# Kernel optimization log

Hardware: AMD Instinct MI355X
Metric: run time of the kernel (lower is better)

Reference implementation:

```python
import jax, jax.numpy as jnp
import numpy as np

N_SRC, N_TGT, K, L, C_OUT = 16384, 16384, 16, 128, 2
E = N_TGT * K
MIN_VAR = 1e-3   # adf.keep_variance_fn min variance (applied in Dropout)
DROP_P = 0.2
INV_SQRT2 = np.float32(1.0 / np.sqrt(2.0))
INV_SQRT2PI = np.float32(1.0 / np.sqrt(2.0 * np.pi))


def setup_inputs() -> dict:
    key = jax.random.key(0)
    ks = jax.random.split(key, 12)
    pos_source = jax.random.uniform(ks[0], (N_SRC, 3), jnp.float32)
    pos_target = jax.random.uniform(ks[1], (N_TGT, 3), jnp.float32)
    latents = jax.random.normal(ks[2], (N_SRC, L), jnp.float32)
    var = jax.random.uniform(ks[3], (N_SRC, L), jnp.float32)
    # KNN-style edge list: each target has K source neighbors
    row = jnp.repeat(jnp.arange(N_TGT, dtype=jnp.int32), K)          # [E] target idx
    col = jax.random.randint(ks[4], (E,), 0, N_SRC, jnp.int32)       # [E] source idx
    occupancies = jax.random.randint(ks[5], (N_TGT,), 0, 2, jnp.int32)
    # fixed inverted-dropout mask (deterministic stand-in for adf.Dropout training mask)
    drop_mask = (jax.random.uniform(ks[6], (E, L)) >= DROP_P).astype(jnp.float32) / (1.0 - DROP_P)
    def init_w(k, sh):
        return jax.random.normal(k, sh, jnp.float32) * np.float32(1.0 / np.sqrt(sh[-1]))
    W_in = init_w(ks[7], (L, L + 3)); b_in = jnp.zeros((L,), jnp.float32)
    W1 = init_w(ks[8], (L, L)); b1 = jnp.zeros((L,), jnp.float32)
    W2 = init_w(ks[9], (L, L)); b2 = jnp.zeros((L,), jnp.float32)
    W_out = init_w(ks[10], (C_OUT, L)); b_out = jnp.zeros((C_OUT,), jnp.float32)
    return dict(pos_source=pos_source, pos_target=pos_target, latents=latents, var=var,
                drop_mask=drop_mask, W_in=W_in, b_in=b_in, W1=W1, b1=b1, W2=W2, b2=b2,
                W_out=W_out, b_out=b_out, row=row, col=col, occupancies=occupancies)


def _adf_linear(m, v, W, b):
    # ADF Linear: mean -> affine; variance -> through squared weights, no bias
    return m @ W.T + b, v @ (W * W).T


def _adf_relu(m, v):
    # ADF ReLU moment matching (Gast & Roth); clamp var for sqrt stability
    v = jnp.maximum(v, 1e-6)
    std = jnp.sqrt(v)
    r = m / std
    cdf = 0.5 * (1.0 + jax.lax.erf(r * INV_SQRT2))
    pdf = jnp.exp(-0.5 * r * r) * INV_SQRT2PI
    m_out = m * cdf + std * pdf
    v_out = (m * m + v) * cdf + m * std * pdf - m_out * m_out
    return m_out, v_out


def reference(pos_source, pos_target, latents, var, drop_mask, W_in, b_in, W1, b1, W2, b2, W_out, b_out, row, col, occupancies):
    pos_rel = pos_target[row] - pos_source[col]                    # [E,3]
    m = jnp.concatenate([latents[col], pos_rel], axis=1)           # [E,L+3]
    v = jnp.concatenate([var[col], pos_rel], axis=1)               # [E,L+3] (faithful: pos_rel reused as 'variance')
    m, v = _adf_linear(m, v, W_in, b_in)
    for W, b in ((W1, b1), (W2, b2)):
        m, v = _adf_relu(m, v)
        m, v = _adf_linear(m, v, W, b)
    # ADF dropout with keep_variance_fn
    m = m * drop_mask
    v = v * drop_mask * drop_mask + MIN_VAR
    m, v = _adf_linear(m, v, W_out, b_out)                         # [E,2]
    preds = m[:, 0]
    aleatoric = jnp.abs(v[:, 0]).mean()
    occ_gt = occupancies[row].astype(jnp.float32)
    # stable binary_cross_entropy_with_logits, mean reduction
    recons_loss = jnp.mean(jnp.maximum(preds, 0.0) - preds * occ_gt + jnp.log1p(jnp.exp(-jnp.abs(preds))))
    return preds, aleatoric, recons_loss, occ_gt
```

## Files before the change

### kernel.cpp

```cpp
#include <hip/hip_runtime.h>
#include <math.h>

#define E_TOT 262144
#define N_SRC 16384
#define LDIM  128
#define XPB   272
#define MIN_VARF 0.001f
#define INV_SQRT2PIF 0.3989422804014327f
#define EPB   128
#define NBLK  (E_TOT / EPB)

typedef _Float16 half8  __attribute__((ext_vector_type(8)));
typedef __fp16   fp16x2 __attribute__((ext_vector_type(2)));
typedef float    f32x4  __attribute__((ext_vector_type(4)));
typedef float    f32x2  __attribute__((ext_vector_type(2)));
typedef unsigned int uint2v __attribute__((ext_vector_type(2)));

#define BIAS_OFF  256
#define WOUT_OFF  1792
#define BOUT_OFF  2816
#define PK_L0     4096
#define PK_L1     45056
#define PK_L2     77824
#define PART_OFF  110592
#define LAT16_OFF 131072
#define VAR16_OFF (LAT16_OFF + N_SRC * LDIM * 2)
#define WS_NEED   (VAR16_OFF + N_SRC * LDIM * 2)

__device__ __forceinline__ unsigned int pkrtz(float a, float b) {
    union { fp16x2 h; unsigned int u; } z;
    z.h = __builtin_amdgcn_cvt_pkrtz(a, b);
    return z.u;
}
__device__ __forceinline__ half8 to_h8(f32x4 a, f32x4 b) {
    union { half8 h; unsigned int u[4]; } z;
    z.u[0] = pkrtz(a[0], a[1]); z.u[1] = pkrtz(a[2], a[3]);
    z.u[2] = pkrtz(b[0], b[1]); z.u[3] = pkrtz(b[2], b[3]);
    return z.h;
}

__device__ __forceinline__ void adf_relu(float& m, float& v) {
    float vv = fmaxf(v, 1e-6f);
    float is = __builtin_amdgcn_rsqf(vv);
    float sd = vv * is;
    float r  = m * is;
    float qq = 0.5f * r * r;
    float e  = __expf(-qq);
    float sp = sd * e * INV_SQRT2PIF;
    const float P = 0.23165247f;
    float t  = __builtin_amdgcn_rcpf(fmaf(fabsf(r), P, 1.0f));
    float poly = t * fmaf(t, fmaf(t, fmaf(t, fmaf(t, 1.061405429f, -1.453152027f),
                                          1.421413741f), -0.284496736f), 0.254829592f);
    float erfa = fmaf(-poly, e, 1.0f);
    float cdf  = fmaf(copysignf(0.5f, r), erfa, 0.5f);
    float mo = fmaf(m, cdf, sp);
    float vo = fmaf(fmaf(m, m, vv), cdf, fmaf(m, sp, -mo * mo));
    m = mo; v = vo;
}

__global__ void prep_pack(const float* __restrict__ latents, const float* __restrict__ varr,
                          char* __restrict__ ws)
{
    int idx = blockIdx.x * 256 + threadIdx.x;
    const int half = idx >> 18;
    const int j    = idx & 262143;
    const float* src = (half ? varr : latents) + (long)j * 8;
    char* dst = ws + (half ? VAR16_OFF : LAT16_OFF) + (long)j * 16;
    f32x4 a = *(const f32x4*)(src);
    f32x4 b = *(const f32x4*)(src + 4);
    half8 hv;
#pragma unroll
    for (int k = 0; k < 4; ++k) { hv[k] = (_Float16)a[k]; hv[k + 4] = (_Float16)b[k]; }
    *(half8*)dst = hv;
}

__global__ void prep(const float* __restrict__ W_in, const float* __restrict__ b_in,
                     const float* __restrict__ W1,   const float* __restrict__ b1,
                     const float* __restrict__ W2,   const float* __restrict__ b2,
                     const float* __restrict__ W_out,const float* __restrict__ b_out,
                     char* __restrict__ ws)
{
    int idx = blockIdx.x * 256 + threadIdx.x;
    if (idx < 6656) {
        const float* W; int Kfull; long dstoff; int entry;
        if (idx < 2560)      { entry = idx;        W = W_in; Kfull = 131; dstoff = PK_L0; }
        else if (idx < 4608) { entry = idx - 2560; W = W1;   Kfull = 128; dstoff = PK_L1; }
        else                 { entry = idx - 4608; W = W2;   Kfull = 128; dstoff = PK_L2; }
        int ks   = entry >> 9;
        int rest = entry & 511;
        int t    = rest >> 6;
        int lane = rest & 63;
        int rowi = t * 16 + (lane & 15);
        int k0   = ks * 32 + (lane >> 4) * 8;
        half8 hv;
#pragma unroll
        for (int j = 0; j < 8; ++j) {
            int k = k0 + j;
            hv[j] = (_Float16)((k < Kfull) ? W[rowi * Kfull + k] : 0.0f);
        }
        *(half8*)(ws + dstoff + (long)entry * 16) = hv;
    } else if (idx < 6656 + 384) {
        int j = idx - 6656; int layer = j >> 7; int pidx = j & 127;
        int gg = pidx >> 5, t = (pidx >> 2) & 7, r = pidx & 3;
        int n = t * 16 + gg * 4 + r;
        const float* b = layer == 0 ? b_in : (layer == 1 ? b1 : b2);
        ((float*)(ws + BIAS_OFF))[layer * 128 + pidx] = b[n];
    } else if (idx < 6656 + 384 + 256) {
        int j = idx - 6656 - 384; int path = j >> 7; int pidx = j & 127;
        int gg = pidx >> 5, t = (pidx >> 2) & 7, r = pidx & 3;
        int n = t * 16 + gg * 4 + r;
        float v = W_out[n];
        if (path) v = v * v;
        ((float*)(ws + WOUT_OFF))[path * 128 + pidx] = v;
    } else if (idx == 6656 + 384 + 256) {
        ((float*)(ws + BOUT_OFF))[0] = b_out[0];
    }
}

__device__ __forceinline__ void epi_store(const f32x4* am, const f32x4* av, const f32x4* bp,
                                          char* xmb, char* xvb, int rowb, int g8)
{
#pragma unroll
    for (int t = 0; t < 8; ++t) {
        f32x4 b4 = bp[t];
        float m0 = am[t][0] + b4[0], m1 = am[t][1] + b4[1];
        float m2 = am[t][2] + b4[2], m3 = am[t][3] + b4[3];
        float v0 = av[t][0], v1 = av[t][1], v2 = av[t][2], v3 = av[t][3];
        adf_relu(m0, v0); adf_relu(m1, v1); adf_relu(m2, v2); adf_relu(m3, v3);
        uint2v sm = {pkrtz(m0, m1), pkrtz(m2, m3)};
        uint2v sv = {pkrtz(v0, v1), pkrtz(v2, v3)};
        *(uint2v*)(xmb + rowb + t * 32 + g8) = sm;
        *(uint2v*)(xvb + rowb + t * 32 + g8) = sv;
    }
}

template <bool PACKED>
__global__ void __launch_bounds__(256, 2)
interp_main(const float* __restrict__ pos_source, const float* __restrict__ pos_target,
            const float* __restrict__ latents,    const float* __restrict__ varr,
            const float* __restrict__ drop_mask,
            const int* __restrict__ row, const int* __restrict__ col, const int* __restrict__ occ,
            float* __restrict__ out, char* __restrict__ ws)
{
    __shared__ __align__(16) short Xm[EPB][XPB / 2];
    __shared__ __align__(16) short Xv[EPB][XPB / 2];
    __shared__ float wred[4][2];

    const int tid  = threadIdx.x;
    const int lane = tid & 63;
    const int w    = tid >> 6;
    const int q    = lane & 15;
    const int g    = lane >> 4;
    const int g8   = g * 8;
    const int er0  = w * 32 + q;
    const int er1  = er0 + 16;
    const int ge0  = blockIdx.x * EPB + er0;
    const int ge1  = ge0 + 16;
    char* xmb = (char*)&Xm[0][0];
    char* xvb = (char*)&Xv[0][0];

    const int c0 = col[ge0], c1 = col[ge1];
    const int r0 = row[ge0], r1 = row[ge1];
    const float occf0 = (float)occ[r0];
    const float occf1 = (float)occ[r1];
    const float px0 = pos_target[r0 * 3 + 0] - pos_source[c0 * 3 + 0];
    const float py0 = pos_target[r0 * 3 + 1] - pos_source[c0 * 3 + 1];
    const float pz0 = pos_target[r0 * 3 + 2] - pos_source[c0 * 3 + 2];
    const float px1 = pos_target[r1 * 3 + 0] - pos_source[c1 * 3 + 0];
    const float py1 = pos_target[r1 * 3 + 1] - pos_source[c1 * 3 + 1];
    const float pz1 = pos_target[r1 * 3 + 2] - pos_source[c1 * 3 + 2];

    f32x4 acm0[8], acv0[8], acm1[8], acv1[8];
    const f32x4 zz = {0.0f, 0.0f, 0.0f, 0.0f};
#pragma unroll
    for (int t = 0; t < 8; ++t) { acm0[t] = zz; acv0[t] = zz; acm1[t] = zz; acv1[t] = zz; }

    {
        const char*  pk  = ws + PK_L0 + lane * 16;
        const char*  l16 = ws + LAT16_OFF;
        const char*  v16 = ws + VAR16_OFF;
        const float* lm0 = latents + (long)c0 * LDIM;
        const float* lv0 = varr    + (long)c0 * LDIM;
        const float* lm1 = latents + (long)c1 * LDIM;
        const float* lv1 = varr    + (long)c1 * LDIM;
#pragma unroll
        for (int ks = 0; ks < 4; ++ks) {
            half8 bm0, bv0, bm1, bv1;
            if (PACKED) {
                const long o0 = (long)c0 * 256 + ks * 64 + g8 * 2;
                const long o1 = (long)c1 * 256 + ks * 64 + g8 * 2;
                bm0 = *(const half8*)(l16 + o0);
                bv0 = *(const half8*)(v16 + o0);
                bm1 = *(const half8*)(l16 + o1);
                bv1 = *(const half8*)(v16 + o1);
            } else {
                const f32x4* a0 = (const f32x4*)(lm0 + ks * 32 + g8);
                const f32x4* s0 = (const f32x4*)(lv0 + ks * 32 + g8);
                const f32x4* a1 = (const f32x4*)(lm1 + ks * 32 + g8);
                const f32x4* s1 = (const f32x4*)(lv1 + ks * 32 + g8);
                bm0 = to_h8(a0[0], a0[1]);
                bv0 = to_h8(s0[0], s0[1]);
                bm1 = to_h8(a1[0], a1[1]);
                bv1 = to_h8(s1[0], s1[1]);
            }
            const char* pmk = pk + ks * 8192;
#pragma unroll
            for (int t = 0; t < 8; ++t) {
                half8 am = *(const half8*)(pmk + t * 1024);
                half8 av = am * am;
                acm0[t] = __builtin_amdgcn_mfma_f32_16x16x32_f16(am, bm0, acm0[t], 0, 0, 0);
                acm1[t] = __builtin_amdgcn_mfma_f32_16x16x32_f16(am, bm1, acm1[t], 0, 0, 0);
                acv0[t] = __builtin_amdgcn_mfma_f32_16x16x32_f16(av, bv0, acv0[t], 0, 0, 0);
                acv1[t] = __builtin_amdgcn_mfma_f32_16x16x32_f16(av, bv1, acv1[t], 0, 0, 0);
            }
        }
        half8 bp0 = {(_Float16)0.f, (_Float16)0.f, (_Float16)0.f, (_Float16)0.f,
                     (_Float16)0.f, (_Float16)0.f, (_Float16)0.f, (_Float16)0.f};
        half8 bp1 = bp0;
        if (g == 0) {
            bp0[0] = (_Float16)px0; bp0[1] = (_Float16)py0; bp0[2] = (_Float16)pz0;
            bp1[0] = (_Float16)px1; bp1[1] = (_Float16)py1; bp1[2] = (_Float16)pz1;
        }
        const char* pmk = pk + 4 * 8192;
#pragma unroll
        for (int t = 0; t < 8; ++t) {
            half8 am = *(const half8*)(pmk + t * 1024);
            half8 av = am * am;
            acm0[t] = __builtin_amdgcn_mfma_f32_16x16x32_f16(am, bp0, acm0[t], 0, 0, 0);
            acm1[t] = __builtin_amdgcn_mfma_f32_16x16x32_f16(am, bp1, acm1[t], 0, 0, 0);
            acv0[t] = __builtin_amdgcn_mfma_f32_16x16x32_f16(av, bp0, acv0[t], 0, 0, 0);
            acv1[t] = __builtin_amdgcn_mfma_f32_16x16x32_f16(av, bp1, acv1[t], 0, 0, 0);
        }
        const f32x4* bp = (const f32x4*)(ws + BIAS_OFF) + g * 8;
        epi_store(acm0, acv0, bp, xmb, xvb, er0 * XPB, g8);
        epi_store(acm1, acv1, bp, xmb, xvb, er1 * XPB, g8);
    }

    for (int layer = 1; layer < 3; ++layer) {
        const char* pk = ws + (layer == 1 ? PK_L1 : PK_L2) + lane * 16;
#pragma unroll
        for (int t = 0; t < 8; ++t) { acm0[t] = zz; acv0[t] = zz; acm1[t] = zz; acv1[t] = zz; }
#pragma unroll
        for (int ks = 0; ks < 4; ++ks) {
            half8 bm0 = *(const half8*)(xmb + er0 * XPB + ks * 64 + g * 16);
            half8 bv0 = *(const half8*)(xvb + er0 * XPB + ks * 64 + g * 16);
            half8 bm1 = *(const half8*)(xmb + er1 * XPB + ks * 64 + g * 16);
            half8 bv1 = *(const half8*)(xvb + er1 * XPB + ks * 64 + g * 16);
            const char* pmk = pk + ks * 8192;
#pragma unroll
            for (int t = 0; t < 8; ++t) {
                half8 am = *(const half8*)(pmk + t * 1024);
                half8 av = am * am;
                acm0[t] = __builtin_amdgcn_mfma_f32_16x16x32_f16(am, bm0, acm0[t], 0, 0, 0);
                acm1[t] = __builtin_amdgcn_mfma_f32_16x16x32_f16(am, bm1, acm1[t], 0, 0, 0);
                acv0[t] = __builtin_amdgcn_mfma_f32_16x16x32_f16(av, bv0, acv0[t], 0, 0, 0);
                acv1[t] = __builtin_amdgcn_mfma_f32_16x16x32_f16(av, bv1, acv1[t], 0, 0, 0);
            }
        }
        if (layer == 1) {
            const f32x4* bp = (const f32x4*)(ws + BIAS_OFF) + 32 + g * 8;
            epi_store(acm0, acv0, bp, xmb, xvb, er0 * XPB, g8);
            epi_store(acm1, acv1, bp, xmb, xvb, er1 * XPB, g8);
        }
    }

    {
        const f32x4* wmp = (const f32x4*)(ws + WOUT_OFF);
        const f32x4* bp  = (const f32x4*)(ws + BIAS_OFF) + 64 + g * 8;
        const f32x4* dm0 = (const f32x4*)(drop_mask + (size_t)ge0 * LDIM) + g;
        const f32x4* dm1 = (const f32x4*)(drop_mask + (size_t)ge1 * LDIM) + g;
        float pm0 = 0.f, pv0 = 0.f, pm1 = 0.f, pv1 = 0.f;
#pragma unroll
        for (int t = 0; t < 8; ++t) {
            f32x4 b4 = bp[t];
            f32x4 w4 = wmp[g * 8 + t];
            f32x4 s4 = wmp[32 + g * 8 + t];
            f32x4 d0 = __builtin_nontemporal_load(dm0 + t * 4);
            f32x4 d1 = __builtin_nontemporal_load(dm1 + t * 4);
#pragma unroll
            for (int j = 0; j < 4; ++j) {
                float m0 = (acm0[t][j] + b4[j]) * d0[j];
                float v0 = acv0[t][j] * d0[j] * d0[j] + MIN_VARF;
                float m1 = (acm1[t][j] + b4[j]) * d1[j];
                float v1 = acv1[t][j] * d1[j] * d1[j] + MIN_VARF;
                pm0 = fmaf(w4[j], m0, pm0); pv0 = fmaf(s4[j], v0, pv0);
                pm1 = fmaf(w4[j], m1, pm1); pv1 = fmaf(s4[j], v1, pv1);
            }
        }
        pm0 += __shfl_xor(pm0, 16, 64); pm0 += __shfl_xor(pm0, 32, 64);
        pv0 += __shfl_xor(pv0, 16, 64); pv0 += __shfl_xor(pv0, 32, 64);
        pm1 += __shfl_xor(pm1, 16, 64); pm1 += __shfl_xor(pm1, 32, 64);
        pv1 += __shfl_xor(pv1, 16, 64); pv1 += __shfl_xor(pv1, 32, 64);
        float bout = *(const float*)(ws + BOUT_OFF);
        float p0 = pm0 + bout;
        float p1 = pm1 + bout;
        if (lane < 16) {
            out[ge0] = p0;            out[ge1] = p1;
            out[E_TOT + 2 + ge0] = occf0;
            out[E_TOT + 2 + ge1] = occf1;
        }
        float a0 = fabsf(p0), a1 = fabsf(p1);
        float loss = fmaxf(p0, 0.f) - p0 * occf0 + __logf(1.0f + __expf(-a0))
                   + fmaxf(p1, 0.f) - p1 * occf1 + __logf(1.0f + __expf(-a1));
        float al = fabsf(pv0) + fabsf(pv1);
#pragma unroll
        for (int off = 1; off < 16; off <<= 1) {
            al   += __shfl_xor(al, off, 64);
            loss += __shfl_xor(loss, off, 64);
        }
        if (lane == 0) { wred[w][0] = al; wred[w][1] = loss; }
    }
    __syncthreads();
    if (tid == 0) {
        f32x2 s;
        s[0] = wred[0][0] + wred[1][0] + wred[2][0] + wred[3][0];
        s[1] = wred[0][1] + wred[1][1] + wred[2][1] + wred[3][1];
        *((f32x2*)(ws + PART_OFF) + blockIdx.x) = s;
    }
}

__global__ void __launch_bounds__(256)
interp_finalize(const char* __restrict__ ws, float* __restrict__ out)
{
    __shared__ float sal[4], sls[4];
    const int tid  = threadIdx.x;
    const int lane = tid & 63;
    const int w    = tid >> 6;
    float al = 0.0f, ls = 0.0f;
    const f32x2* part = (const f32x2*)(ws + PART_OFF);
    for (int i = tid; i < NBLK; i += 256) {
        f32x2 p = part[i];
        al += p[0]; ls += p[1];
    }
#pragma unroll
    for (int off = 1; off < 64; off <<= 1) {
        al += __shfl_xor(al, off, 64);
        ls += __shfl_xor(ls, off, 64);
    }
    if (lane == 0) { sal[w] = al; sls[w] = ls; }
    __syncthreads();
    if (tid == 0) {
        const float inv = 1.0f / (float)E_TOT;
        out[E_TOT]     = (sal[0] + sal[1] + sal[2] + sal[3]) * inv;
        out[E_TOT + 1] = (sls[0] + sls[1] + sls[2] + sls[3]) * inv;
    }
}

extern "C" void kernel_launch(void* const* d_in, const int* in_sizes, int n_in,
                              void* d_out, int out_size, void* d_ws, size_t ws_size,
                              hipStream_t stream) {
    (void)in_sizes; (void)n_in; (void)out_size;
    const float* pos_source = (const float*)d_in[0];
    const float* pos_target = (const float*)d_in[1];
    const float* latents    = (const float*)d_in[2];
    const float* varr       = (const float*)d_in[3];
    const float* drop_mask  = (const float*)d_in[4];
    const float* W_in       = (const float*)d_in[5];
    const float* b_in       = (const float*)d_in[6];
    const float* W1         = (const float*)d_in[7];
    const float* b1         = (const float*)d_in[8];
    const float* W2         = (const float*)d_in[9];
    const float* b2         = (const float*)d_in[10];
    const float* W_out      = (const float*)d_in[11];
    const float* b_out      = (const float*)d_in[12];
    const int*   row        = (const int*)d_in[13];
    const int*   col        = (const int*)d_in[14];
    const int*   occ        = (const int*)d_in[15];
    float* out = (float*)d_out;
    char*  ws  = (char*)d_ws;

    const bool packed = (ws_size >= (size_t)WS_NEED);
    prep<<<29, 256, 0, stream>>>(W_in, b_in, W1, b1, W2, b2, W_out, b_out, ws);
    if (packed) {
        prep_pack<<<2048, 256, 0, stream>>>(latents, varr, ws);
        interp_main<true><<<NBLK, 256, 0, stream>>>(
            pos_source, pos_target, latents, varr, drop_mask,
            row, col, occ, out, ws);
    } else {
        interp_main<false><<<NBLK, 256, 0, stream>>>(
            pos_source, pos_target, latents, varr, drop_mask,
            row, col, occ, out, ws);
    }
    interp_finalize<<<1, 256, 0, stream>>>(ws, out);
}
```

Baseline: 148.1 us.

## Keep inter-layer activations in registers instead of LDS, halve edges per wave

Hidden activations no longer make a round trip through LDS between layers. Instead, layers 1 and 2 are given a K-permuted weight packing so that the MFMA accumulator layout of one layer directly forms the B operand of the next, and the packed fp16 results stay in registers. Each wave now handles 16 edges instead of 32, with 64 edges per block, and launch bounds go from 2 to 3 blocks per SM to raise occupancy. This removes the LDS stores, loads and shared memory footprint. In exchange, each weight fragment loaded from global/L2 is reused across half as many MFMAs, so weight traffic per edge doubles.

```diff
diff --git a/kernel.cpp b/kernel.cpp
--- a/kernel.cpp
+++ b/kernel.cpp
@@ -4,10 +4,9 @@
 #define E_TOT 262144
 #define N_SRC 16384
 #define LDIM  128
-#define XPB   272
 #define MIN_VARF 0.001f
 #define INV_SQRT2PIF 0.3989422804014327f
-#define EPB   128
+#define EPB   64
 #define NBLK  (E_TOT / EPB)
 
 typedef _Float16 half8  __attribute__((ext_vector_type(8)));
@@ -19,13 +18,13 @@
 #define BIAS_OFF  256
 #define WOUT_OFF  1792
 #define BOUT_OFF  2816
-#define PK_L0     4096
-#define PK_L1     45056
-#define PK_L2     77824
-#define PART_OFF  110592
-#define LAT16_OFF 131072
-#define VAR16_OFF (LAT16_OFF + N_SRC * LDIM * 2)
-#define WS_NEED   (VAR16_OFF + N_SRC * LDIM * 2)
+#define PART_OFF  4096
+#define PK_L0     36864
+#define PK_L1     77824
+#define PK_L2     110592
+#define LAT16_OFF 143360
+#define VAR16_OFF 4337664
+#define WS_NEED   8531968
 
 __device__ __forceinline__ unsigned int pkrtz(float a, float b) {
     union { fp16x2 h; unsigned int u; } z;
@@ -36,6 +35,11 @@
     union { half8 h; unsigned int u[4]; } z;
     z.u[0] = pkrtz(a[0], a[1]); z.u[1] = pkrtz(a[2], a[3]);
     z.u[2] = pkrtz(b[0], b[1]); z.u[3] = pkrtz(b[2], b[3]);
+    return z.h;
+}
+__device__ __forceinline__ half8 ch_to_h8(uint2v lo, uint2v hi) {
+    union { half8 h; unsigned int u[4]; } z;
+    z.u[0] = lo[0]; z.u[1] = lo[1]; z.u[2] = hi[0]; z.u[3] = hi[1];
     return z.h;
 }
 
@@ -82,21 +86,30 @@
 {
     int idx = blockIdx.x * 256 + threadIdx.x;
     if (idx < 6656) {
-        const float* W; int Kfull; long dstoff; int entry;
-        if (idx < 2560)      { entry = idx;        W = W_in; Kfull = 131; dstoff = PK_L0; }
-        else if (idx < 4608) { entry = idx - 2560; W = W1;   Kfull = 128; dstoff = PK_L1; }
-        else                 { entry = idx - 4608; W = W2;   Kfull = 128; dstoff = PK_L2; }
+        const float* W; long dstoff; int entry; bool lin;
+        if (idx < 2560)      { entry = idx;        W = W_in; dstoff = PK_L0; lin = true;  }
+        else if (idx < 4608) { entry = idx - 2560; W = W1;   dstoff = PK_L1; lin = false; }
+        else                 { entry = idx - 4608; W = W2;   dstoff = PK_L2; lin = false; }
         int ks   = entry >> 9;
         int rest = entry & 511;
         int t    = rest >> 6;
         int lane = rest & 63;
         int rowi = t * 16 + (lane & 15);
-        int k0   = ks * 32 + (lane >> 4) * 8;
+        int gp   = lane >> 4;
         half8 hv;
-#pragma unroll
-        for (int j = 0; j < 8; ++j) {
-            int k = k0 + j;
-            hv[j] = (_Float16)((k < Kfull) ? W[rowi * Kfull + k] : 0.0f);
+        if (lin) {
+            int k0 = ks * 32 + gp * 8;
+#pragma unroll
+            for (int j = 0; j < 8; ++j) {
+                int k = k0 + j;
+                hv[j] = (_Float16)((k < 131) ? W[rowi * 131 + k] : 0.0f);
+            }
+        } else {
+#pragma unroll
+            for (int j = 0; j < 8; ++j) {
+                int k = (2 * ks + (j >= 4 ? 1 : 0)) * 16 + 4 * gp + (j & 3);
+                hv[j] = (_Float16)W[rowi * 128 + k];
+            }
         }
         *(half8*)(ws + dstoff + (long)entry * 16) = hv;
     } else if (idx < 6656 + 384) {
@@ -117,8 +130,8 @@
     }
 }
 
-__device__ __forceinline__ void epi_store(const f32x4* am, const f32x4* av, const f32x4* bp,
-                                          char* xmb, char* xvb, int rowb, int g8)
+__device__ __forceinline__ void epi_reg(const f32x4* am, const f32x4* av, const f32x4* bp,
+                                        uint2v* chm, uint2v* chv)
 {
 #pragma unroll
     for (int t = 0; t < 8; ++t) {
@@ -129,21 +142,18 @@
         adf_relu(m0, v0); adf_relu(m1, v1); adf_relu(m2, v2); adf_relu(m3, v3);
         uint2v sm = {pkrtz(m0, m1), pkrtz(m2, m3)};
         uint2v sv = {pkrtz(v0, v1), pkrtz(v2, v3)};
-        *(uint2v*)(xmb + rowb + t * 32 + g8) = sm;
-        *(uint2v*)(xvb + rowb + t * 32 + g8) = sv;
+        chm[t] = sm; chv[t] = sv;
     }
 }
 
 template <bool PACKED>
-__global__ void __launch_bounds__(256, 2)
+__global__ void __launch_bounds__(256, 3)
 interp_main(const float* __restrict__ pos_source, const float* __restrict__ pos_target,
             const float* __restrict__ latents,    const float* __restrict__ varr,
             const float* __restrict__ drop_mask,
             const int* __restrict__ row, const int* __restrict__ col, const int* __restrict__ occ,
             float* __restrict__ out, char* __restrict__ ws)
 {
-    __shared__ __align__(16) short Xm[EPB][XPB / 2];
-    __shared__ __align__(16) short Xv[EPB][XPB / 2];
     __shared__ float wred[4][2];
 
     const int tid  = threadIdx.x;
@@ -152,157 +162,113 @@
     const int q    = lane & 15;
     const int g    = lane >> 4;
     const int g8   = g * 8;
-    const int er0  = w * 32 + q;
-    const int er1  = er0 + 16;
-    const int ge0  = blockIdx.x * EPB + er0;
-    const int ge1  = ge0 + 16;
-    char* xmb = (char*)&Xm[0][0];
-    char* xvb = (char*)&Xv[0][0];
-
-    const int c0 = col[ge0], c1 = col[ge1];
-    const int r0 = row[ge0], r1 = row[ge1];
-    const float occf0 = (float)occ[r0];
-    const float occf1 = (float)occ[r1];
-    const float px0 = pos_target[r0 * 3 + 0] - pos_source[c0 * 3 + 0];
-    const float py0 = pos_target[r0 * 3 + 1] - pos_source[c0 * 3 + 1];
-    const float pz0 = pos_target[r0 * 3 + 2] - pos_source[c0 * 3 + 2];
-    const float px1 = pos_target[r1 * 3 + 0] - pos_source[c1 * 3 + 0];
-    const float py1 = pos_target[r1 * 3 + 1] - pos_source[c1 * 3 + 1];
-    const float pz1 = pos_target[r1 * 3 + 2] - pos_source[c1 * 3 + 2];
-
-    f32x4 acm0[8], acv0[8], acm1[8], acv1[8];
+    const int er   = w * 16 + q;
+    const int ge   = blockIdx.x * EPB + er;
+    (void)q;
+
+    const int c0 = col[ge];
+    const int r0 = row[ge];
+    const float occf = (float)occ[r0];
+    const float px = pos_target[r0 * 3 + 0] - pos_source[c0 * 3 + 0];
+    const float py = pos_target[r0 * 3 + 1] - pos_source[c0 * 3 + 1];
+    const float pz = pos_target[r0 * 3 + 2] - pos_source[c0 * 3 + 2];
+
+    f32x4 acm[8], acv[8];
     const f32x4 zz = {0.0f, 0.0f, 0.0f, 0.0f};
 #pragma unroll
-    for (int t = 0; t < 8; ++t) { acm0[t] = zz; acv0[t] = zz; acm1[t] = zz; acv1[t] = zz; }
+    for (int t = 0; t < 8; ++t) { acm[t] = zz; acv[t] = zz; }
+
+    uint2v chm[8], chv[8];
 
     {
-        const char*  pk  = ws + PK_L0 + lane * 16;
-        const char*  l16 = ws + LAT16_OFF;
-        const char*  v16 = ws + VAR16_OFF;
-        const float* lm0 = latents + (long)c0 * LDIM;
-        const float* lv0 = varr    + (long)c0 * LDIM;
-        const float* lm1 = latents + (long)c1 * LDIM;
-        const float* lv1 = varr    + (long)c1 * LDIM;
+        const char* pk = ws + PK_L0 + lane * 16;
 #pragma unroll
         for (int ks = 0; ks < 4; ++ks) {
-            half8 bm0, bv0, bm1, bv1;
+            half8 bm, bv;
             if (PACKED) {
                 const long o0 = (long)c0 * 256 + ks * 64 + g8 * 2;
-                const long o1 = (long)c1 * 256 + ks * 64 + g8 * 2;
-                bm0 = *(const half8*)(l16 + o0);
-                bv0 = *(const half8*)(v16 + o0);
-                bm1 = *(const half8*)(l16 + o1);
-                bv1 = *(const half8*)(v16 + o1);
+                bm = *(const half8*)(ws + LAT16_OFF + o0);
+                bv = *(const half8*)(ws + VAR16_OFF + o0);
             } else {
-                const f32x4* a0 = (const f32x4*)(lm0 + ks * 32 + g8);
-                const f32x4* s0 = (const f32x4*)(lv0 + ks * 32 + g8);
-                const f32x4* a1 = (const f32x4*)(lm1 + ks * 32 + g8);
-                const f32x4* s1 = (const f32x4*)(lv1 + ks * 32 + g8);
-                bm0 = to_h8(a0[0], a0[1]);
-                bv0 = to_h8(s0[0], s0[1]);
-                bm1 = to_h8(a1[0], a1[1]);
-                bv1 = to_h8(s1[0], s1[1]);
+                const f32x4* a0 = (const f32x4*)(latents + (long)c0 * LDIM + ks * 32 + g8);
+                const f32x4* s0 = (const f32x4*)(varr    + (long)c0 * LDIM + ks * 32 + g8);
+                bm = to_h8(a0[0], a0[1]);
+                bv = to_h8(s0[0], s0[1]);
             }
             const char* pmk = pk + ks * 8192;
 #pragma unroll
             for (int t = 0; t < 8; ++t) {
                 half8 am = *(const half8*)(pmk + t * 1024);
                 half8 av = am * am;
-                acm0[t] = __builtin_amdgcn_mfma_f32_16x16x32_f16(am, bm0, acm0[t], 0, 0, 0);
-                acm1[t] = __builtin_amdgcn_mfma_f32_16x16x32_f16(am, bm1, acm1[t], 0, 0, 0);
-                acv0[t] = __builtin_amdgcn_mfma_f32_16x16x32_f16(av, bv0, acv0[t], 0, 0, 0);
-                acv1[t] = __builtin_amdgcn_mfma_f32_16x16x32_f16(av, bv1, acv1[t], 0, 0, 0);
-            }
-        }
-        half8 bp0 = {(_Float16)0.f, (_Float16)0.f, (_Float16)0.f, (_Float16)0.f,
-                     (_Float16)0.f, (_Float16)0.f, (_Float16)0.f, (_Float16)0.f};
-        half8 bp1 = bp0;
-        if (g == 0) {
-            bp0[0] = (_Float16)px0; bp0[1] = (_Float16)py0; bp0[2] = (_Float16)pz0;
-            bp1[0] = (_Float16)px1; bp1[1] = (_Float16)py1; bp1[2] = (_Float16)pz1;
-        }
+                acm[t] = __builtin_amdgcn_mfma_f32_16x16x32_f16(am, bm, acm[t], 0, 0, 0);
+                acv[t] = __builtin_amdgcn_mfma_f32_16x16x32_f16(av, bv, acv[t], 0, 0, 0);
+            }
+        }
+        half8 bpos = {(_Float16)0.f, (_Float16)0.f, (_Float16)0.f, (_Float16)0.f,
+                      (_Float16)0.f, (_Float16)0.f, (_Float16)0.f, (_Float16)0.f};
+        if (g == 0) { bpos[0] = (_Float16)px; bpos[1] = (_Float16)py; bpos[2] = (_Float16)pz; }
         const char* pmk = pk + 4 * 8192;
 #pragma unroll
         for (int t = 0; t < 8; ++t) {
             half8 am = *(const half8*)(pmk + t * 1024);
             half8 av = am * am;
-            acm0[t] = __builtin_amdgcn_mfma_f32_16x16x32_f16(am, bp0, acm0[t], 0, 0, 0);
-            acm1[t] = __builtin_amdgcn_mfma_f32_16x16x32_f16(am, bp1, acm1[t], 0, 0, 0);
-            acv0[t] = __builtin_amdgcn_mfma_f32_16x16x32_f16(av, bp0, acv0[t], 0, 0, 0);
-            acv1[t] = __builtin_amdgcn_mfma_f32_16x16x32_f16(av, bp1, acv1[t], 0, 0, 0);
-        }
-        const f32x4* bp = (const f32x4*)(ws + BIAS_OFF) + g * 8;
-        epi_store(acm0, acv0, bp, xmb, xvb, er0 * XPB, g8);
-        epi_store(acm1, acv1, bp, xmb, xvb, er1 * XPB, g8);
-    }
-
+            acm[t] = __builtin_amdgcn_mfma_f32_16x16x32_f16(am, bpos, acm[t], 0, 0, 0);
+            acv[t] = __builtin_amdgcn_mfma_f32_16x16x32_f16(av, bpos, acv[t], 0, 0, 0);
+        }
+        epi_reg(acm, acv, (const f32x4*)(ws + BIAS_OFF) + g8, chm, chv);
+    }
+
+#pragma unroll
     for (int layer = 1; layer < 3; ++layer) {
         const char* pk = ws + (layer == 1 ? PK_L1 : PK_L2) + lane * 16;
 #pragma unroll
-        for (int t = 0; t < 8; ++t) { acm0[t] = zz; acv0[t] = zz; acm1[t] = zz; acv1[t] = zz; }
+        for (int t = 0; t < 8; ++t) { acm[t] = zz; acv[t] = zz; }
 #pragma unroll
         for (int ks = 0; ks < 4; ++ks) {
-            half8 bm0 = *(const half8*)(xmb + er0 * XPB + ks * 64 + g * 16);
-            half8 bv0 = *(const half8*)(xvb + er0 * XPB + ks * 64 + g * 16);
-            half8 bm1 = *(const half8*)(xmb + er1 * XPB + ks * 64 + g * 16);
-            half8 bv1 = *(const half8*)(xvb + er1 * XPB + ks * 64 + g * 16);
+            half8 bm = ch_to_h8(chm[2 * ks], chm[2 * ks + 1]);
+            half8 bv = ch_to_h8(chv[2 * ks], chv[2 * ks + 1]);
             const char* pmk = pk + ks * 8192;
 #pragma unroll
             for (int t = 0; t < 8; ++t) {
                 half8 am = *(const half8*)(pmk + t * 1024);
                 half8 av = am * am;
-                acm0[t] = __builtin_amdgcn_mfma_f32_16x16x32_f16(am, bm0, acm0[t], 0, 0, 0);
-                acm1[t] = __builtin_amdgcn_mfma_f32_16x16x32_f16(am, bm1, acm1[t], 0, 0, 0);
-                acv0[t] = __builtin_amdgcn_mfma_f32_16x16x32_f16(av, bv0, acv0[t], 0, 0, 0);
-                acv1[t] = __builtin_amdgcn_mfma_f32_16x16x32_f16(av, bv1, acv1[t], 0, 0, 0);
-            }
-        }
-        if (layer == 1) {
-            const f32x4* bp = (const f32x4*)(ws + BIAS_OFF) + 32 + g * 8;
-            epi_store(acm0, acv0, bp, xmb, xvb, er0 * XPB, g8);
-            epi_store(acm1, acv1, bp, xmb, xvb, er1 * XPB, g8);
-        }
+                acm[t] = __builtin_amdgcn_mfma_f32_16x16x32_f16(am, bm, acm[t], 0, 0, 0);
+                acv[t] = __builtin_amdgcn_mfma_f32_16x16x32_f16(av, bv, acv[t], 0, 0, 0);
+            }
+        }
+        if (layer == 1)
+            epi_reg(acm, acv, (const f32x4*)(ws + BIAS_OFF) + 32 + g8, chm, chv);
     }
 
     {
         const f32x4* wmp = (const f32x4*)(ws + WOUT_OFF);
-        const f32x4* bp  = (const f32x4*)(ws + BIAS_OFF) + 64 + g * 8;
-        const f32x4* dm0 = (const f32x4*)(drop_mask + (size_t)ge0 * LDIM) + g;
-        const f32x4* dm1 = (const f32x4*)(drop_mask + (size_t)ge1 * LDIM) + g;
-        float pm0 = 0.f, pv0 = 0.f, pm1 = 0.f, pv1 = 0.f;
+        const f32x4* bp  = (const f32x4*)(ws + BIAS_OFF) + 64 + g8;
+        const f32x4* dmp = (const f32x4*)(drop_mask + (size_t)ge * LDIM) + g;
+        float pm = 0.f, pv = 0.f;
 #pragma unroll
         for (int t = 0; t < 8; ++t) {
             f32x4 b4 = bp[t];
-            f32x4 w4 = wmp[g * 8 + t];
-            f32x4 s4 = wmp[32 + g * 8 + t];
-            f32x4 d0 = __builtin_nontemporal_load(dm0 + t * 4);
-            f32x4 d1 = __builtin_nontemporal_load(dm1 + t * 4);
+            f32x4 w4 = wmp[g8 + t];
+            f32x4 s4 = wmp[32 + g8 + t];
+            f32x4 d4 = __builtin_nontemporal_load(dmp + t * 4);
 #pragma unroll
             for (int j = 0; j < 4; ++j) {
-                float m0 = (acm0[t][j] + b4[j]) * d0[j];
-                float v0 = acv0[t][j] * d0[j] * d0[j] + MIN_VARF;
-                float m1 = (acm1[t][j] + b4[j]) * d1[j];
-                float v1 = acv1[t][j] * d1[j] * d1[j] + MIN_VARF;
-                pm0 = fmaf(w4[j], m0, pm0); pv0 = fmaf(s4[j], v0, pv0);
-                pm1 = fmaf(w4[j], m1, pm1); pv1 = fmaf(s4[j], v1, pv1);
-            }
-        }
-        pm0 += __shfl_xor(pm0, 16, 64); pm0 += __shfl_xor(pm0, 32, 64);
-        pv0 += __shfl_xor(pv0, 16, 64); pv0 += __shfl_xor(pv0, 32, 64);
-        pm1 += __shfl_xor(pm1, 16, 64); pm1 += __shfl_xor(pm1, 32, 64);
-        pv1 += __shfl_xor(pv1, 16, 64); pv1 += __shfl_xor(pv1, 32, 64);
+                float m0 = (acm[t][j] + b4[j]) * d4[j];
+                float v0 = acv[t][j] * d4[j] * d4[j] + MIN_VARF;
+                pm = fmaf(w4[j], m0, pm); pv = fmaf(s4[j], v0, pv);
+            }
+        }
+        pm += __shfl_xor(pm, 16, 64); pm += __shfl_xor(pm, 32, 64);
+        pv += __shfl_xor(pv, 16, 64); pv += __shfl_xor(pv, 32, 64);
         float bout = *(const float*)(ws + BOUT_OFF);
-        float p0 = pm0 + bout;
-        float p1 = pm1 + bout;
+        float p = pm + bout;
         if (lane < 16) {
-            out[ge0] = p0;            out[ge1] = p1;
-            out[E_TOT + 2 + ge0] = occf0;
-            out[E_TOT + 2 + ge1] = occf1;
-        }
-        float a0 = fabsf(p0), a1 = fabsf(p1);
-        float loss = fmaxf(p0, 0.f) - p0 * occf0 + __logf(1.0f + __expf(-a0))
-                   + fmaxf(p1, 0.f) - p1 * occf1 + __logf(1.0f + __expf(-a1));
-        float al = fabsf(pv0) + fabsf(pv1);
+            out[ge] = p;
+            out[E_TOT + 2 + ge] = occf;
+        }
+        float a = fabsf(p);
+        float loss = fmaxf(p, 0.f) - p * occf + __logf(1.0f + __expf(-a));
+        float al = fabsf(pv);
 #pragma unroll
         for (int off = 1; off < 16; off <<= 1) {
             al   += __shfl_xor(al, off, 64);
```

Result: slower. 221.3 us (+49.4%).

## Keep inter-layer activations in registers by permuting packed weight K order

Applied to the files above, without the earlier changes.

Hidden-layer weights are now packed in a permuted K order, so each lane's MFMA accumulator outputs (after ReLU and fp16 packing) line up with the B-operand fragment it needs for the next layer. Intermediate activations therefore stay in registers instead of going through roughly 68KB of shared memory per block, which removes LDS stores and loads and the shared-memory footprint. The cost is 32 extra packed registers per thread holding activation chunks, which raises register pressure. The layer loop is also fully unrolled and the workspace offsets are rearranged.

```diff
diff --git a/kernel.cpp b/kernel.cpp
--- a/kernel.cpp
+++ b/kernel.cpp
@@ -4,7 +4,6 @@
 #define E_TOT 262144
 #define N_SRC 16384
 #define LDIM  128
-#define XPB   272
 #define MIN_VARF 0.001f
 #define INV_SQRT2PIF 0.3989422804014327f
 #define EPB   128
@@ -19,13 +18,13 @@
 #define BIAS_OFF  256
 #define WOUT_OFF  1792
 #define BOUT_OFF  2816
-#define PK_L0     4096
-#define PK_L1     45056
-#define PK_L2     77824
-#define PART_OFF  110592
-#define LAT16_OFF 131072
-#define VAR16_OFF (LAT16_OFF + N_SRC * LDIM * 2)
-#define WS_NEED   (VAR16_OFF + N_SRC * LDIM * 2)
+#define PART_OFF  4096
+#define PK_L0     36864
+#define PK_L1     77824
+#define PK_L2     110592
+#define LAT16_OFF 143360
+#define VAR16_OFF 4337664
+#define WS_NEED   8531968
 
 __device__ __forceinline__ unsigned int pkrtz(float a, float b) {
     union { fp16x2 h; unsigned int u; } z;
@@ -36,6 +35,11 @@
     union { half8 h; unsigned int u[4]; } z;
     z.u[0] = pkrtz(a[0], a[1]); z.u[1] = pkrtz(a[2], a[3]);
     z.u[2] = pkrtz(b[0], b[1]); z.u[3] = pkrtz(b[2], b[3]);
+    return z.h;
+}
+__device__ __forceinline__ half8 ch_to_h8(uint2v lo, uint2v hi) {
+    union { half8 h; unsigned int u[4]; } z;
+    z.u[0] = lo[0]; z.u[1] = lo[1]; z.u[2] = hi[0]; z.u[3] = hi[1];
     return z.h;
 }
 
@@ -82,21 +86,30 @@
 {
     int idx = blockIdx.x * 256 + threadIdx.x;
     if (idx < 6656) {
-        const float* W; int Kfull; long dstoff; int entry;
-        if (idx < 2560)      { entry = idx;        W = W_in; Kfull = 131; dstoff = PK_L0; }
-        else if (idx < 4608) { entry = idx - 2560; W = W1;   Kfull = 128; dstoff = PK_L1; }
-        else                 { entry = idx - 4608; W = W2;   Kfull = 128; dstoff = PK_L2; }
+        const float* W; long dstoff; int entry; bool lin;
+        if (idx < 2560)      { entry = idx;        W = W_in; dstoff = PK_L0; lin = true;  }
+        else if (idx < 4608) { entry = idx - 2560; W = W1;   dstoff = PK_L1; lin = false; }
+        else                 { entry = idx - 4608; W = W2;   dstoff = PK_L2; lin = false; }
         int ks   = entry >> 9;
         int rest = entry & 511;
         int t    = rest >> 6;
         int lane = rest & 63;
         int rowi = t * 16 + (lane & 15);
-        int k0   = ks * 32 + (lane >> 4) * 8;
+        int gp   = lane >> 4;
         half8 hv;
-#pragma unroll
-        for (int j = 0; j < 8; ++j) {
-            int k = k0 + j;
-            hv[j] = (_Float16)((k < Kfull) ? W[rowi * Kfull + k] : 0.0f);
+        if (lin) {
+            int k0 = ks * 32 + gp * 8;
+#pragma unroll
+            for (int j = 0; j < 8; ++j) {
+                int k = k0 + j;
+                hv[j] = (_Float16)((k < 131) ? W[rowi * 131 + k] : 0.0f);
+            }
+        } else {
+#pragma unroll
+            for (int j = 0; j < 8; ++j) {
+                int k = (2 * ks + (j >= 4 ? 1 : 0)) * 16 + 4 * gp + (j & 3);
+                hv[j] = (_Float16)W[rowi * 128 + k];
+            }
         }
         *(half8*)(ws + dstoff + (long)entry * 16) = hv;
     } else if (idx < 6656 + 384) {
@@ -117,8 +130,8 @@
     }
 }
 
-__device__ __forceinline__ void epi_store(const f32x4* am, const f32x4* av, const f32x4* bp,
-                                          char* xmb, char* xvb, int rowb, int g8)
+__device__ __forceinline__ void epi_reg(const f32x4* am, const f32x4* av, const f32x4* bp,
+                                        uint2v* chm, uint2v* chv)
 {
 #pragma unroll
     for (int t = 0; t < 8; ++t) {
@@ -129,8 +142,7 @@
         adf_relu(m0, v0); adf_relu(m1, v1); adf_relu(m2, v2); adf_relu(m3, v3);
         uint2v sm = {pkrtz(m0, m1), pkrtz(m2, m3)};
         uint2v sv = {pkrtz(v0, v1), pkrtz(v2, v3)};
-        *(uint2v*)(xmb + rowb + t * 32 + g8) = sm;
-        *(uint2v*)(xvb + rowb + t * 32 + g8) = sv;
+        chm[t] = sm; chv[t] = sv;
     }
 }
 
@@ -142,8 +154,6 @@
             const int* __restrict__ row, const int* __restrict__ col, const int* __restrict__ occ,
             float* __restrict__ out, char* __restrict__ ws)
 {
-    __shared__ __align__(16) short Xm[EPB][XPB / 2];
-    __shared__ __align__(16) short Xv[EPB][XPB / 2];
     __shared__ float wred[4][2];
 
     const int tid  = threadIdx.x;
@@ -156,8 +166,6 @@
     const int er1  = er0 + 16;
     const int ge0  = blockIdx.x * EPB + er0;
     const int ge1  = ge0 + 16;
-    char* xmb = (char*)&Xm[0][0];
-    char* xvb = (char*)&Xv[0][0];
 
     const int c0 = col[ge0], c1 = col[ge1];
     const int r0 = row[ge0], r1 = row[ge1];
@@ -175,33 +183,27 @@
 #pragma unroll
     for (int t = 0; t < 8; ++t) { acm0[t] = zz; acv0[t] = zz; acm1[t] = zz; acv1[t] = zz; }
 
+    uint2v chm0[8], chv0[8], chm1[8], chv1[8];
+
     {
-        const char*  pk  = ws + PK_L0 + lane * 16;
-        const char*  l16 = ws + LAT16_OFF;
-        const char*  v16 = ws + VAR16_OFF;
-        const float* lm0 = latents + (long)c0 * LDIM;
-        const float* lv0 = varr    + (long)c0 * LDIM;
-        const float* lm1 = latents + (long)c1 * LDIM;
-        const float* lv1 = varr    + (long)c1 * LDIM;
+        const char* pk = ws + PK_L0 + lane * 16;
 #pragma unroll
         for (int ks = 0; ks < 4; ++ks) {
             half8 bm0, bv0, bm1, bv1;
             if (PACKED) {
                 const long o0 = (long)c0 * 256 + ks * 64 + g8 * 2;
                 const long o1 = (long)c1 * 256 + ks * 64 + g8 * 2;
-                bm0 = *(const half8*)(l16 + o0);
-                bv0 = *(const half8*)(v16 + o0);
-                bm1 = *(const half8*)(l16 + o1);
-                bv1 = *(const half8*)(v16 + o1);
+                bm0 = *(const half8*)(ws + LAT16_OFF + o0);
+                bv0 = *(const half8*)(ws + VAR16_OFF + o0);
+                bm1 = *(const half8*)(ws + LAT16_OFF + o1);
+                bv1 = *(const half8*)(ws + VAR16_OFF + o1);
             } else {
-                const f32x4* a0 = (const f32x4*)(lm0 + ks * 32 + g8);
-                const f32x4* s0 = (const f32x4*)(lv0 + ks * 32 + g8);
-                const f32x4* a1 = (const f32x4*)(lm1 + ks * 32 + g8);
-                const f32x4* s1 = (const f32x4*)(lv1 + ks * 32 + g8);
-                bm0 = to_h8(a0[0], a0[1]);
-                bv0 = to_h8(s0[0], s0[1]);
-                bm1 = to_h8(a1[0], a1[1]);
-                bv1 = to_h8(s1[0], s1[1]);
+                const f32x4* a0 = (const f32x4*)(latents + (long)c0 * LDIM + ks * 32 + g8);
+                const f32x4* s0 = (const f32x4*)(varr    + (long)c0 * LDIM + ks * 32 + g8);
+                const f32x4* a1 = (const f32x4*)(latents + (long)c1 * LDIM + ks * 32 + g8);
+                const f32x4* s1 = (const f32x4*)(varr    + (long)c1 * LDIM + ks * 32 + g8);
+                bm0 = to_h8(a0[0], a0[1]); bv0 = to_h8(s0[0], s0[1]);
+                bm1 = to_h8(a1[0], a1[1]); bv1 = to_h8(s1[0], s1[1]);
             }
             const char* pmk = pk + ks * 8192;
 #pragma unroll
@@ -231,21 +233,22 @@
             acv0[t] = __builtin_amdgcn_mfma_f32_16x16x32_f16(av, bp0, acv0[t], 0, 0, 0);
             acv1[t] = __builtin_amdgcn_mfma_f32_16x16x32_f16(av, bp1, acv1[t], 0, 0, 0);
         }
-        const f32x4* bp = (const f32x4*)(ws + BIAS_OFF) + g * 8;
-        epi_store(acm0, acv0, bp, xmb, xvb, er0 * XPB, g8);
-        epi_store(acm1, acv1, bp, xmb, xvb, er1 * XPB, g8);
-    }
-
+        const f32x4* bp = (const f32x4*)(ws + BIAS_OFF) + g8;
+        epi_reg(acm0, acv0, bp, chm0, chv0);
+        epi_reg(acm1, acv1, bp, chm1, chv1);
+    }
+
+#pragma unroll
     for (int layer = 1; layer < 3; ++layer) {
         const char* pk = ws + (layer == 1 ? PK_L1 : PK_L2) + lane * 16;
 #pragma unroll
         for (int t = 0; t < 8; ++t) { acm0[t] = zz; acv0[t] = zz; acm1[t] = zz; acv1[t] = zz; }
 #pragma unroll
         for (int ks = 0; ks < 4; ++ks) {
-            half8 bm0 = *(const half8*)(xmb + er0 * XPB + ks * 64 + g * 16);
-            half8 bv0 = *(const half8*)(xvb + er0 * XPB + ks * 64 + g * 16);
-            half8 bm1 = *(const half8*)(xmb + er1 * XPB + ks * 64 + g * 16);
-            half8 bv1 = *(const half8*)(xvb + er1 * XPB + ks * 64 + g * 16);
+            half8 bm0 = ch_to_h8(chm0[2 * ks], chm0[2 * ks + 1]);
+            half8 bv0 = ch_to_h8(chv0[2 * ks], chv0[2 * ks + 1]);
+            half8 bm1 = ch_to_h8(chm1[2 * ks], chm1[2 * ks + 1]);
+            half8 bv1 = ch_to_h8(chv1[2 * ks], chv1[2 * ks + 1]);
             const char* pmk = pk + ks * 8192;
 #pragma unroll
             for (int t = 0; t < 8; ++t) {
@@ -258,23 +261,23 @@
             }
         }
         if (layer == 1) {
-            const f32x4* bp = (const f32x4*)(ws + BIAS_OFF) + 32 + g * 8;
-            epi_store(acm0, acv0, bp, xmb, xvb, er0 * XPB, g8);
-            epi_store(acm1, acv1, bp, xmb, xvb, er1 * XPB, g8);
+            const f32x4* bp = (const f32x4*)(ws + BIAS_OFF) + 32 + g8;
+            epi_reg(acm0, acv0, bp, chm0, chv0);
+            epi_reg(acm1, acv1, bp, chm1, chv1);
         }
     }
 
     {
         const f32x4* wmp = (const f32x4*)(ws + WOUT_OFF);
-        const f32x4* bp  = (const f32x4*)(ws + BIAS_OFF) + 64 + g * 8;
+        const f32x4* bp  = (const f32x4*)(ws + BIAS_OFF) + 64 + g8;
         const f32x4* dm0 = (const f32x4*)(drop_mask + (size_t)ge0 * LDIM) + g;
         const f32x4* dm1 = (const f32x4*)(drop_mask + (size_t)ge1 * LDIM) + g;
         float pm0 = 0.f, pv0 = 0.f, pm1 = 0.f, pv1 = 0.f;
 #pragma unroll
         for (int t = 0; t < 8; ++t) {
             f32x4 b4 = bp[t];
-            f32x4 w4 = wmp[g * 8 + t];
-            f32x4 s4 = wmp[32 + g * 8 + t];
+            f32x4 w4 = wmp[g8 + t];
+            f32x4 s4 = wmp[32 + g8 + t];
             f32x4 d0 = __builtin_nontemporal_load(dm0 + t * 4);
             f32x4 d1 = __builtin_nontemporal_load(dm1 + t * 4);
 #pragma unroll
```

Measured after the change: 144.9 us. 2.1% less time.
